# Optimization experiments

Hardware: AMD Instinct MI355X
Metric: run time of the kernel (lower is better)

The kernel has to match this reference:

```python
import jax, jax.numpy as jnp
import numpy as np

H = 1024
NH = 16
HD = H // NH  # 64


def setup_inputs() -> dict:
    key = jax.random.key(0)
    ks = jax.random.split(key, 7)
    s = 1.0 / np.sqrt(H)
    return {
        "hidden_states": jax.random.normal(ks[0], (4, 2048, H), dtype=jnp.float32),
        "Wq": jax.random.normal(ks[1], (H, H), dtype=jnp.float32) * s,
        "bq": jnp.zeros((H,), dtype=jnp.float32),
        "Wk": jax.random.normal(ks[2], (H, H), dtype=jnp.float32) * s,
        "bk": jnp.zeros((H,), dtype=jnp.float32),
        "Wv": jax.random.normal(ks[3], (H, H), dtype=jnp.float32) * s,
        "bv": jnp.zeros((H,), dtype=jnp.float32),
    }


def _split_heads(x):
    # [B,S,H] -> [B,NH,S,HD]
    b, s, _ = x.shape
    return x.reshape(b, s, NH, HD).transpose(0, 2, 1, 3)


def reference(hidden_states, Wq, bq, Wk, bk, Wv, bv):
    q = _split_heads(hidden_states @ Wq + bq)
    k = _split_heads(hidden_states @ Wk + bk)
    v = _split_heads(hidden_states @ Wv + bv)
    scores = jnp.einsum("bhqd,bhkd->bhqk", q, k) / jnp.sqrt(jnp.float32(HD))
    probs = jax.nn.softmax(scores, axis=-1)  # dropout p=0 (eval) -> identity
    ctx = jnp.einsum("bhqk,bhkd->bhqd", probs, v)
    b, _, s, _ = ctx.shape
    return ctx.transpose(0, 2, 1, 3).reshape(b, s, H)
```

## Files before the change

### kernel.cpp

```cpp
#include <hip/hip_runtime.h>
#include <hip/hip_bf16.h>

#define BB  4
#define SS  2048
#define HH  1024
#define NHH 16
#define HDD 64

typedef unsigned short u16;
typedef unsigned int   u32;
using bf16x8 = __attribute__((ext_vector_type(8))) short;
using f32x4  = __attribute__((ext_vector_type(4))) float;
using f32x16 = __attribute__((ext_vector_type(16))) float;
using u32x4  = __attribute__((ext_vector_type(4))) u32;

__device__ __forceinline__ u16 f2b(float f) {
    union { float f; u32 u; } x; x.f = f;
    return (u16)((x.u + 0x7fffu + ((x.u >> 16) & 1u)) >> 16);
}

__device__ __forceinline__ void gload16(const u16* g, u16* l) {
    __builtin_amdgcn_global_load_lds(
        (const __attribute__((address_space(1))) void*)g,
        (__attribute__((address_space(3))) void*)l, 16, 0, 0);
}

__global__ __launch_bounds__(256) void conv(
    const float* __restrict__ X,
    const float* __restrict__ Wq, const float* __restrict__ Wk,
    const float* __restrict__ Wv,
    u16* __restrict__ Xb, u16* __restrict__ Wt)
{
    const int bid = blockIdx.x;
    const int t = threadIdx.x;
    if (bid < 4096) {
        const int i = bid * 256 + t;
        float4 a = ((const float4*)X)[i * 2];
        float4 b = ((const float4*)X)[i * 2 + 1];
        ushort4 s0, s1;
        s0.x = f2b(a.x); s0.y = f2b(a.y); s0.z = f2b(a.z); s0.w = f2b(a.w);
        s1.x = f2b(b.x); s1.y = f2b(b.y); s1.z = f2b(b.z); s1.w = f2b(b.w);
        ((ushort4*)Xb)[i * 2] = s0;
        ((ushort4*)Xb)[i * 2 + 1] = s1;
        return;
    }
    const int idx = bid - 4096;
    const int z = idx >> 10, rem = idx & 1023;
    const int k0 = (rem >> 5) * 32, n0 = (rem & 31) * 32;
    const float* W = (z == 0) ? Wq : (z == 1) ? Wk : Wv;
    u16* out = Wt + (size_t)z * HH * HH;
    __shared__ float T[32][33];
    {
        const int kl = t >> 3, n4 = (t & 7) * 4;
        float4 v = *(const float4*)&W[(size_t)(k0 + kl) * HH + n0 + n4];
        T[n4 + 0][kl] = v.x; T[n4 + 1][kl] = v.y;
        T[n4 + 2][kl] = v.z; T[n4 + 3][kl] = v.w;
    }
    __syncthreads();
    {
        const int nl = t >> 3, k4 = (t & 7) * 4;
        ushort4 s;
        s.x = f2b(T[nl][k4 + 0]); s.y = f2b(T[nl][k4 + 1]);
        s.z = f2b(T[nl][k4 + 2]); s.w = f2b(T[nl][k4 + 3]);
        *(ushort4*)&out[(size_t)(n0 + nl) * HH + k0 + k4] = s;
    }
}

__global__ __launch_bounds__(256) void qkv_gemm(
    const u16* __restrict__ Xb, const u16* __restrict__ Wtb,
    const float* __restrict__ bq, const float* __restrict__ bk,
    const float* __restrict__ bv,
    u16* __restrict__ Qw, u16* __restrict__ Kw, u16* __restrict__ Vw)
{
    const int z  = blockIdx.z;
    const float* bias = (z == 0) ? bq : (z == 1) ? bk : bv;
    const int m0 = blockIdx.x * 128, n0 = blockIdx.y * 128;

    __shared__ __align__(16) u16 Xs[128 * 64];
    __shared__ __align__(16) u16 Ws[128 * 64];

    const int t = threadIdx.x;
    const int w = t >> 6, lane = t & 63, lr = lane & 15, quad = lane >> 4;
    const int l3 = lane >> 3, c7 = lane & 7;
    const int cl = (c7 ^ l3) * 8;
    const int wm = w >> 1, wn = w & 1;

    const u16* Wtz = Wtb + (size_t)z * HH * HH;

    f32x4 acc[4][4];
    #pragma unroll
    for (int i = 0; i < 4; i++)
        #pragma unroll
        for (int j = 0; j < 4; j++) acc[i][j] = f32x4{0.f, 0.f, 0.f, 0.f};

    for (int k0 = 0; k0 < HH; k0 += 64) {
        #pragma unroll
        for (int e = 0; e < 4; e++) {
            const int r = w * 32 + e * 8 + l3;
            gload16(&Xb [(size_t)(m0 + r) * HH + k0 + cl], &Xs[(w * 32 + e * 8) * 64]);
            gload16(&Wtz[(size_t)(n0 + r) * HH + k0 + cl], &Ws[(w * 32 + e * 8) * 64]);
        }
        __syncthreads();

        #pragma unroll
        for (int kc = 0; kc < 2; kc++) {
            bf16x8 af[4], bfr[4];
            const int ph = ((kc * 4 + quad) ^ c7) * 8;
            #pragma unroll
            for (int mi = 0; mi < 4; mi++)
                af[mi] = *(const bf16x8*)&Xs[(wm * 64 + mi * 16 + lr) * 64 + ph];
            #pragma unroll
            for (int ni = 0; ni < 4; ni++)
                bfr[ni] = *(const bf16x8*)&Ws[(wn * 64 + ni * 16 + lr) * 64 + ph];
            if (z != 2) {
                #pragma unroll
                for (int mi = 0; mi < 4; mi++)
                    #pragma unroll
                    for (int ni = 0; ni < 4; ni++)
                        acc[mi][ni] = __builtin_amdgcn_mfma_f32_16x16x32_bf16(
                            bfr[ni], af[mi], acc[mi][ni], 0, 0, 0);
            } else {
                #pragma unroll
                for (int mi = 0; mi < 4; mi++)
                    #pragma unroll
                    for (int ni = 0; ni < 4; ni++)
                        acc[mi][ni] = __builtin_amdgcn_mfma_f32_16x16x32_bf16(
                            af[mi], bfr[ni], acc[mi][ni], 0, 0, 0);
            }
        }
        __syncthreads();
    }

    if (z != 2) {
        u16* dst = (z == 0) ? Qw : Kw;
        const float cs = (z == 0) ? 0.18033688011112042f : 1.0f;
        #pragma unroll
        for (int mi = 0; mi < 4; mi++) {
            const int sg = m0 + wm * 64 + mi * 16 + lr;
            const int b = sg >> 11, s = sg & 2047;
            #pragma unroll
            for (int ni = 0; ni < 4; ni++) {
                const int nb = n0 + wn * 64 + ni * 16 + quad * 4;
                const int h = nb >> 6, d0 = nb & 63;
                float4 bb4 = *(const float4*)&bias[nb];
                ushort4 vs;
                vs.x = f2b((acc[mi][ni][0] + bb4.x) * cs);
                vs.y = f2b((acc[mi][ni][1] + bb4.y) * cs);
                vs.z = f2b((acc[mi][ni][2] + bb4.z) * cs);
                vs.w = f2b((acc[mi][ni][3] + bb4.w) * cs);
                *(ushort4*)&dst[((size_t)(b * NHH + h) * SS + s) * HDD + d0] = vs;
            }
        }
    } else {
        #pragma unroll
        for (int mi = 0; mi < 4; mi++)
            #pragma unroll
            for (int ni = 0; ni < 4; ni++) {
                const int mb = m0 + wm * 64 + mi * 16 + quad * 4;
                const int b = mb >> 11, s0 = mb & 2047;
                const int n = n0 + wn * 64 + ni * 16 + lr;
                const int h = n >> 6, d = n & 63;
                const float bv4 = bias[n];
                ushort4 vs;
                vs.x = f2b(acc[mi][ni][0] + bv4);
                vs.y = f2b(acc[mi][ni][1] + bv4);
                vs.z = f2b(acc[mi][ni][2] + bv4);
                vs.w = f2b(acc[mi][ni][3] + bv4);
                *(ushort4*)&Vw[((size_t)(b * NHH + h) * HDD + d) * SS + s0] = vs;
            }
    }
}

struct PU { union { u32x4 u; bf16x8 v; }; };

__device__ __forceinline__ void packP(const f32x16& s0, const f32x16& s1,
                                      PU pa[4], float& lsum) {
    #pragma unroll
    for (int kb = 0; kb < 2; kb++) {
        const f32x16& s = kb ? s1 : s0;
        float p[16];
        #pragma unroll
        for (int r = 0; r < 16; r++) p[r] = __builtin_amdgcn_exp2f(s[r]);
        lsum += ((((p[0] + p[1]) + (p[2] + p[3]))
                + ((p[4] + p[5]) + (p[6] + p[7])))
               + (((p[8] + p[9]) + (p[10] + p[11]))
                + ((p[12] + p[13]) + (p[14] + p[15]))));
        u32 x0, x1, x2, x3, y0, y1, y2, y3;
        asm("v_cvt_pk_bf16_f32 %0, %1, %2" : "=v"(x0) : "v"(p[0]),  "v"(p[1]));
        asm("v_cvt_pk_bf16_f32 %0, %1, %2" : "=v"(x1) : "v"(p[2]),  "v"(p[3]));
        asm("v_cvt_pk_bf16_f32 %0, %1, %2" : "=v"(y0) : "v"(p[4]),  "v"(p[5]));
        asm("v_cvt_pk_bf16_f32 %0, %1, %2" : "=v"(y1) : "v"(p[6]),  "v"(p[7]));
        asm("v_cvt_pk_bf16_f32 %0, %1, %2" : "=v"(x2) : "v"(p[8]),  "v"(p[9]));
        asm("v_cvt_pk_bf16_f32 %0, %1, %2" : "=v"(x3) : "v"(p[10]), "v"(p[11]));
        asm("v_cvt_pk_bf16_f32 %0, %1, %2" : "=v"(y2) : "v"(p[12]), "v"(p[13]));
        asm("v_cvt_pk_bf16_f32 %0, %1, %2" : "=v"(y3) : "v"(p[14]), "v"(p[15]));
        asm("v_permlane32_swap_b32 %0, %1" : "+v"(x0), "+v"(y0));
        asm("v_permlane32_swap_b32 %0, %1" : "+v"(x1), "+v"(y1));
        asm("v_permlane32_swap_b32 %0, %1" : "+v"(x2), "+v"(y2));
        asm("v_permlane32_swap_b32 %0, %1" : "+v"(x3), "+v"(y3));
        pa[kb * 2 + 0].u = u32x4{x0, x1, y0, y1};
        pa[kb * 2 + 1].u = u32x4{x2, x3, y2, y3};
    }
}

__global__ __launch_bounds__(256, 2) void attn(
    const u16* __restrict__ Qb, const u16* __restrict__ Kb,
    const u16* __restrict__ Vtb, float* __restrict__ Out)
{
    const int bid = blockIdx.x;
    const int hh = bid & 63, qt = bid >> 6;
    const int b = hh >> 4, h = hh & 15;
    const size_t hb = (size_t)hh * SS * HDD;

    __shared__ __align__(16) u16 Ks[2][64 * 64];
    __shared__ __align__(16) u16 Vs[2][64 * 64];

    const int t = threadIdx.x;
    const int w = t >> 6, lane = t & 63;
    const int q32 = lane & 31, hi = lane >> 5;
    const int l3 = lane >> 3, c7 = lane & 7;
    const int cl = (c7 ^ l3) * 8;

    bf16x8 qfA[4], qfB[4];
    {
        const size_t qrA = (size_t)(qt * 256 + w * 64 + q32);
        #pragma unroll
        for (int ds = 0; ds < 4; ds++) {
            qfA[ds] = *(const bf16x8*)&Qb[hb + qrA * HDD + ds * 16 + hi * 8];
            qfB[ds] = *(const bf16x8*)&Qb[hb + (qrA + 32) * HDD + ds * 16 + hi * 8];
        }
    }

    {
        const int r0 = w * 16 + l3, r1 = r0 + 8;
        gload16(&Kb [hb + (size_t)r0 * HDD + cl], &Ks[0][(w * 16) * 64]);
        gload16(&Kb [hb + (size_t)r1 * HDD + cl], &Ks[0][(w * 16 + 8) * 64]);
        gload16(&Vtb[hb + (size_t)r0 * SS + cl],  &Vs[0][(w * 16) * 64]);
        gload16(&Vtb[hb + (size_t)r1 * SS + cl],  &Vs[0][(w * 16 + 8) * 64]);
    }
    __syncthreads();

    float lsA = 0.f, lsB = 0.f;
    f32x16 oA0 = {}, oA1 = {}, oB0 = {}, oB1 = {};

    for (int kt = 0; kt < SS / 64; kt++) {
        const int bb = kt & 1;
        if (kt + 1 < SS / 64) {
            const int r0 = w * 16 + l3, r1 = r0 + 8;
            gload16(&Kb [hb + (size_t)((kt + 1) * 64 + r0) * HDD + cl],
                    &Ks[bb ^ 1][(w * 16) * 64]);
            gload16(&Kb [hb + (size_t)((kt + 1) * 64 + r1) * HDD + cl],
                    &Ks[bb ^ 1][(w * 16 + 8) * 64]);
            gload16(&Vtb[hb + (size_t)r0 * SS + (kt + 1) * 64 + cl],
                    &Vs[bb ^ 1][(w * 16) * 64]);
            gload16(&Vtb[hb + (size_t)r1 * SS + (kt + 1) * 64 + cl],
                    &Vs[bb ^ 1][(w * 16 + 8) * 64]);
        }

        f32x16 sA0 = {}, sA1 = {}, sB0 = {}, sB1 = {};
        __builtin_amdgcn_s_setprio(1);
        #pragma unroll
        for (int ds = 0; ds < 4; ds++) {
            const int ph = ((ds * 2 + hi) ^ c7) * 8;
            bf16x8 kf0 = *(const bf16x8*)&Ks[bb][q32 * 64 + ph];
            bf16x8 kf1 = *(const bf16x8*)&Ks[bb][(32 + q32) * 64 + ph];
            sA0 = __builtin_amdgcn_mfma_f32_32x32x16_bf16(kf0, qfA[ds], sA0, 0, 0, 0);
            sA1 = __builtin_amdgcn_mfma_f32_32x32x16_bf16(kf1, qfA[ds], sA1, 0, 0, 0);
            sB0 = __builtin_amdgcn_mfma_f32_32x32x16_bf16(kf0, qfB[ds], sB0, 0, 0, 0);
            sB1 = __builtin_amdgcn_mfma_f32_32x32x16_bf16(kf1, qfB[ds], sB1, 0, 0, 0);
        }
        __builtin_amdgcn_s_setprio(0);

        PU paA[4], paB[4];
        packP(sA0, sA1, paA, lsA);
        packP(sB0, sB1, paB, lsB);

        __builtin_amdgcn_s_setprio(1);
        #pragma unroll
        for (int ks = 0; ks < 4; ks++) {
            const int ph = ((ks * 2 + hi) ^ c7) * 8;
            bf16x8 vf0 = *(const bf16x8*)&Vs[bb][q32 * 64 + ph];
            bf16x8 vf1 = *(const bf16x8*)&Vs[bb][(32 + q32) * 64 + ph];
            oA0 = __builtin_amdgcn_mfma_f32_32x32x16_bf16(paA[ks].v, vf0, oA0, 0, 0, 0);
            oA1 = __builtin_amdgcn_mfma_f32_32x32x16_bf16(paA[ks].v, vf1, oA1, 0, 0, 0);
            oB0 = __builtin_amdgcn_mfma_f32_32x32x16_bf16(paB[ks].v, vf0, oB0, 0, 0, 0);
            oB1 = __builtin_amdgcn_mfma_f32_32x32x16_bf16(paB[ks].v, vf1, oB1, 0, 0, 0);
        }
        __builtin_amdgcn_s_setprio(0);
        __syncthreads();
    }

    lsA += __shfl_xor(lsA, 32);
    lsB += __shfl_xor(lsB, 32);
    const float invA = 1.0f / lsA, invB = 1.0f / lsB;

    #pragma unroll
    for (int r = 0; r < 16; r++) {
        const int cr = (r & 3) + 8 * (r >> 2) + 4 * hi;
        const float iA = __shfl(invA, cr);
        const float iB = __shfl(invB, cr);
        const int rqA = qt * 256 + w * 64 + cr;
        float* oA = &Out[((size_t)(b * SS + rqA)) * HH + h * HDD + q32];
        oA[0]  = oA0[r] * iA;
        oA[32] = oA1[r] * iA;
        float* oB = &Out[((size_t)(b * SS + rqA + 32)) * HH + h * HDD + q32];
        oB[0]  = oB0[r] * iB;
        oB[32] = oB1[r] * iB;
    }
}

extern "C" void kernel_launch(void* const* d_in, const int* in_sizes, int n_in,
                              void* d_out, int out_size, void* d_ws, size_t ws_size,
                              hipStream_t stream) {
    const float* X  = (const float*)d_in[0];
    const float* Wq = (const float*)d_in[1];
    const float* bq = (const float*)d_in[2];
    const float* Wk = (const float*)d_in[3];
    const float* bk = (const float*)d_in[4];
    const float* Wv = (const float*)d_in[5];
    const float* bv = (const float*)d_in[6];
    float* Out = (float*)d_out;

    const size_t elems = (size_t)BB * SS * HH;
    u16* Qw = (u16*)d_ws;
    u16* Kw = Qw + elems;
    u16* Vw = Kw + elems;
    u16* Xb = (u16*)d_out;
    u16* Wt = Xb + elems;

    conv<<<dim3(4096 + 3072), 256, 0, stream>>>(X, Wq, Wk, Wv, Xb, Wt);
    qkv_gemm<<<dim3(64, 8, 3), 256, 0, stream>>>(Xb, Wt, bq, bk, bv, Qw, Kw, Vw);
    attn<<<dim3(512), 256, 0, stream>>>(Qw, Kw, Vw, Out);
}
```

Measured before the change: 243.5 us.

## Double-buffer QKV GEMM and split attention softmax into interleaved halves

The QKV GEMM gets double-buffered LDS tiles with prefetch of the next k-slice. Each full __syncthreads is replaced by an explicit vmcnt wait plus s_barrier, so the load in flight is not drained at every step. In attention, the score and PV MFMAs are split into two halves so the exp/pack work of one half can overlap MFMA work of the other, and the same partial vmcnt waits are used. This adds 32KB of LDS to the GEMM, relies on hand-counted vmcnt values that must match the number of loads issued, and uses sched barriers that constrain the compiler's scheduling.

```diff
diff --git a/kernel.cpp b/kernel.cpp
--- a/kernel.cpp
+++ b/kernel.cpp
@@ -13,6 +13,12 @@
 using f32x4  = __attribute__((ext_vector_type(4))) float;
 using f32x16 = __attribute__((ext_vector_type(16))) float;
 using u32x4  = __attribute__((ext_vector_type(4))) u32;
+
+#define SBAR()   asm volatile("s_barrier" ::: "memory")
+#define WAITV0() asm volatile("s_waitcnt vmcnt(0)" ::: "memory")
+#define WAITV4() asm volatile("s_waitcnt vmcnt(4)" ::: "memory")
+#define WAITV8() asm volatile("s_waitcnt vmcnt(8)" ::: "memory")
+#define SCHEDB() __builtin_amdgcn_sched_barrier(0)
 
 __device__ __forceinline__ u16 f2b(float f) {
     union { float f; u32 u; } x; x.f = f;
@@ -66,7 +72,7 @@
     }
 }
 
-__global__ __launch_bounds__(256) void qkv_gemm(
+__global__ __launch_bounds__(256, 2) void qkv_gemm(
     const u16* __restrict__ Xb, const u16* __restrict__ Wtb,
     const float* __restrict__ bq, const float* __restrict__ bk,
     const float* __restrict__ bv,
@@ -76,8 +82,8 @@
     const float* bias = (z == 0) ? bq : (z == 1) ? bk : bv;
     const int m0 = blockIdx.x * 128, n0 = blockIdx.y * 128;
 
-    __shared__ __align__(16) u16 Xs[128 * 64];
-    __shared__ __align__(16) u16 Ws[128 * 64];
+    __shared__ __align__(16) u16 Xs[2][128 * 64];
+    __shared__ __align__(16) u16 Ws[2][128 * 64];
 
     const int t = threadIdx.x;
     const int w = t >> 6, lane = t & 63, lr = lane & 15, quad = lane >> 4;
@@ -93,14 +99,31 @@
         #pragma unroll
         for (int j = 0; j < 4; j++) acc[i][j] = f32x4{0.f, 0.f, 0.f, 0.f};
 
-    for (int k0 = 0; k0 < HH; k0 += 64) {
-        #pragma unroll
-        for (int e = 0; e < 4; e++) {
-            const int r = w * 32 + e * 8 + l3;
-            gload16(&Xb [(size_t)(m0 + r) * HH + k0 + cl], &Xs[(w * 32 + e * 8) * 64]);
-            gload16(&Wtz[(size_t)(n0 + r) * HH + k0 + cl], &Ws[(w * 32 + e * 8) * 64]);
-        }
-        __syncthreads();
+    #pragma unroll
+    for (int e = 0; e < 4; e++) {
+        const int r = w * 32 + e * 8 + l3;
+        gload16(&Xb [(size_t)(m0 + r) * HH + cl], &Xs[0][(w * 32 + e * 8) * 64]);
+        gload16(&Wtz[(size_t)(n0 + r) * HH + cl], &Ws[0][(w * 32 + e * 8) * 64]);
+    }
+
+    for (int kt = 0; kt < 16; kt++) {
+        const int cur = kt & 1;
+        if (kt < 15) {
+            const int k0 = (kt + 1) * 64;
+            #pragma unroll
+            for (int e = 0; e < 4; e++) {
+                const int r = w * 32 + e * 8 + l3;
+                gload16(&Xb [(size_t)(m0 + r) * HH + k0 + cl],
+                        &Xs[cur ^ 1][(w * 32 + e * 8) * 64]);
+                gload16(&Wtz[(size_t)(n0 + r) * HH + k0 + cl],
+                        &Ws[cur ^ 1][(w * 32 + e * 8) * 64]);
+            }
+            WAITV8();
+        } else {
+            WAITV0();
+        }
+        SBAR();
+        SCHEDB();
 
         #pragma unroll
         for (int kc = 0; kc < 2; kc++) {
@@ -108,10 +131,10 @@
             const int ph = ((kc * 4 + quad) ^ c7) * 8;
             #pragma unroll
             for (int mi = 0; mi < 4; mi++)
-                af[mi] = *(const bf16x8*)&Xs[(wm * 64 + mi * 16 + lr) * 64 + ph];
+                af[mi] = *(const bf16x8*)&Xs[cur][(wm * 64 + mi * 16 + lr) * 64 + ph];
             #pragma unroll
             for (int ni = 0; ni < 4; ni++)
-                bfr[ni] = *(const bf16x8*)&Ws[(wn * 64 + ni * 16 + lr) * 64 + ph];
+                bfr[ni] = *(const bf16x8*)&Ws[cur][(wn * 64 + ni * 16 + lr) * 64 + ph];
             if (z != 2) {
                 #pragma unroll
                 for (int mi = 0; mi < 4; mi++)
@@ -128,7 +151,8 @@
                             af[mi], bfr[ni], acc[mi][ni], 0, 0, 0);
             }
         }
-        __syncthreads();
+        SCHEDB();
+        SBAR();
     }
 
     if (z != 2) {
@@ -173,34 +197,29 @@
 
 struct PU { union { u32x4 u; bf16x8 v; }; };
 
-__device__ __forceinline__ void packP(const f32x16& s0, const f32x16& s1,
-                                      PU pa[4], float& lsum) {
+__device__ __forceinline__ void packHalf(const f32x16& s, PU* pa, float& lsum) {
+    float p[16];
     #pragma unroll
-    for (int kb = 0; kb < 2; kb++) {
-        const f32x16& s = kb ? s1 : s0;
-        float p[16];
-        #pragma unroll
-        for (int r = 0; r < 16; r++) p[r] = __builtin_amdgcn_exp2f(s[r]);
-        lsum += ((((p[0] + p[1]) + (p[2] + p[3]))
-                + ((p[4] + p[5]) + (p[6] + p[7])))
-               + (((p[8] + p[9]) + (p[10] + p[11]))
-                + ((p[12] + p[13]) + (p[14] + p[15]))));
-        u32 x0, x1, x2, x3, y0, y1, y2, y3;
-        asm("v_cvt_pk_bf16_f32 %0, %1, %2" : "=v"(x0) : "v"(p[0]),  "v"(p[1]));
-        asm("v_cvt_pk_bf16_f32 %0, %1, %2" : "=v"(x1) : "v"(p[2]),  "v"(p[3]));
-        asm("v_cvt_pk_bf16_f32 %0, %1, %2" : "=v"(y0) : "v"(p[4]),  "v"(p[5]));
-        asm("v_cvt_pk_bf16_f32 %0, %1, %2" : "=v"(y1) : "v"(p[6]),  "v"(p[7]));
-        asm("v_cvt_pk_bf16_f32 %0, %1, %2" : "=v"(x2) : "v"(p[8]),  "v"(p[9]));
-        asm("v_cvt_pk_bf16_f32 %0, %1, %2" : "=v"(x3) : "v"(p[10]), "v"(p[11]));
-        asm("v_cvt_pk_bf16_f32 %0, %1, %2" : "=v"(y2) : "v"(p[12]), "v"(p[13]));
-        asm("v_cvt_pk_bf16_f32 %0, %1, %2" : "=v"(y3) : "v"(p[14]), "v"(p[15]));
-        asm("v_permlane32_swap_b32 %0, %1" : "+v"(x0), "+v"(y0));
-        asm("v_permlane32_swap_b32 %0, %1" : "+v"(x1), "+v"(y1));
-        asm("v_permlane32_swap_b32 %0, %1" : "+v"(x2), "+v"(y2));
-        asm("v_permlane32_swap_b32 %0, %1" : "+v"(x3), "+v"(y3));
-        pa[kb * 2 + 0].u = u32x4{x0, x1, y0, y1};
-        pa[kb * 2 + 1].u = u32x4{x2, x3, y2, y3};
-    }
+    for (int r = 0; r < 16; r++) p[r] = __builtin_amdgcn_exp2f(s[r]);
+    lsum += ((((p[0] + p[1]) + (p[2] + p[3]))
+            + ((p[4] + p[5]) + (p[6] + p[7])))
+           + (((p[8] + p[9]) + (p[10] + p[11]))
+            + ((p[12] + p[13]) + (p[14] + p[15]))));
+    u32 x0, x1, x2, x3, y0, y1, y2, y3;
+    asm("v_cvt_pk_bf16_f32 %0, %1, %2" : "=v"(x0) : "v"(p[0]),  "v"(p[1]));
+    asm("v_cvt_pk_bf16_f32 %0, %1, %2" : "=v"(x1) : "v"(p[2]),  "v"(p[3]));
+    asm("v_cvt_pk_bf16_f32 %0, %1, %2" : "=v"(y0) : "v"(p[4]),  "v"(p[5]));
+    asm("v_cvt_pk_bf16_f32 %0, %1, %2" : "=v"(y1) : "v"(p[6]),  "v"(p[7]));
+    asm("v_cvt_pk_bf16_f32 %0, %1, %2" : "=v"(x2) : "v"(p[8]),  "v"(p[9]));
+    asm("v_cvt_pk_bf16_f32 %0, %1, %2" : "=v"(x3) : "v"(p[10]), "v"(p[11]));
+    asm("v_cvt_pk_bf16_f32 %0, %1, %2" : "=v"(y2) : "v"(p[12]), "v"(p[13]));
+    asm("v_cvt_pk_bf16_f32 %0, %1, %2" : "=v"(y3) : "v"(p[14]), "v"(p[15]));
+    asm("v_permlane32_swap_b32 %0, %1" : "+v"(x0), "+v"(y0));
+    asm("v_permlane32_swap_b32 %0, %1" : "+v"(x1), "+v"(y1));
+    asm("v_permlane32_swap_b32 %0, %1" : "+v"(x2), "+v"(y2));
+    asm("v_permlane32_swap_b32 %0, %1" : "+v"(x3), "+v"(y3));
+    pa[0].u = u32x4{x0, x1, y0, y1};
+    pa[1].u = u32x4{x2, x3, y2, y3};
 }
 
 __global__ __launch_bounds__(256, 2) void attn(
@@ -230,6 +249,8 @@
             qfB[ds] = *(const bf16x8*)&Qb[hb + (qrA + 32) * HDD + ds * 16 + hi * 8];
         }
     }
+    asm volatile("" :: "v"(qfA[0]), "v"(qfA[1]), "v"(qfA[2]), "v"(qfA[3]),
+                       "v"(qfB[0]), "v"(qfB[1]), "v"(qfB[2]), "v"(qfB[3]));
 
     {
         const int r0 = w * 16 + l3, r1 = r0 + 8;
@@ -238,7 +259,6 @@
         gload16(&Vtb[hb + (size_t)r0 * SS + cl],  &Vs[0][(w * 16) * 64]);
         gload16(&Vtb[hb + (size_t)r1 * SS + cl],  &Vs[0][(w * 16 + 8) * 64]);
     }
-    __syncthreads();
 
     float lsA = 0.f, lsB = 0.f;
     f32x16 oA0 = {}, oA1 = {}, oB0 = {}, oB1 = {};
@@ -255,29 +275,39 @@
                     &Vs[bb ^ 1][(w * 16) * 64]);
             gload16(&Vtb[hb + (size_t)r1 * SS + (kt + 1) * 64 + cl],
                     &Vs[bb ^ 1][(w * 16 + 8) * 64]);
-        }
-
-        f32x16 sA0 = {}, sA1 = {}, sB0 = {}, sB1 = {};
+            WAITV4();
+        } else {
+            WAITV0();
+        }
+        SBAR();
+        SCHEDB();
+
+        f32x16 sA0 = {}, sB0 = {};
         __builtin_amdgcn_s_setprio(1);
         #pragma unroll
         for (int ds = 0; ds < 4; ds++) {
             const int ph = ((ds * 2 + hi) ^ c7) * 8;
-            bf16x8 kf0 = *(const bf16x8*)&Ks[bb][q32 * 64 + ph];
-            bf16x8 kf1 = *(const bf16x8*)&Ks[bb][(32 + q32) * 64 + ph];
-            sA0 = __builtin_amdgcn_mfma_f32_32x32x16_bf16(kf0, qfA[ds], sA0, 0, 0, 0);
-            sA1 = __builtin_amdgcn_mfma_f32_32x32x16_bf16(kf1, qfA[ds], sA1, 0, 0, 0);
-            sB0 = __builtin_amdgcn_mfma_f32_32x32x16_bf16(kf0, qfB[ds], sB0, 0, 0, 0);
-            sB1 = __builtin_amdgcn_mfma_f32_32x32x16_bf16(kf1, qfB[ds], sB1, 0, 0, 0);
+            bf16x8 kf = *(const bf16x8*)&Ks[bb][q32 * 64 + ph];
+            sA0 = __builtin_amdgcn_mfma_f32_32x32x16_bf16(kf, qfA[ds], sA0, 0, 0, 0);
+            sB0 = __builtin_amdgcn_mfma_f32_32x32x16_bf16(kf, qfB[ds], sB0, 0, 0, 0);
+        }
+        f32x16 sA1 = {}, sB1 = {};
+        #pragma unroll
+        for (int ds = 0; ds < 4; ds++) {
+            const int ph = ((ds * 2 + hi) ^ c7) * 8;
+            bf16x8 kf = *(const bf16x8*)&Ks[bb][(32 + q32) * 64 + ph];
+            sA1 = __builtin_amdgcn_mfma_f32_32x32x16_bf16(kf, qfA[ds], sA1, 0, 0, 0);
+            sB1 = __builtin_amdgcn_mfma_f32_32x32x16_bf16(kf, qfB[ds], sB1, 0, 0, 0);
         }
         __builtin_amdgcn_s_setprio(0);
 
         PU paA[4], paB[4];
-        packP(sA0, sA1, paA, lsA);
-        packP(sB0, sB1, paB, lsB);
+        packHalf(sA0, &paA[0], lsA);
+        packHalf(sB0, &paB[0], lsB);
 
         __builtin_amdgcn_s_setprio(1);
         #pragma unroll
-        for (int ks = 0; ks < 4; ks++) {
+        for (int ks = 0; ks < 2; ks++) {
             const int ph = ((ks * 2 + hi) ^ c7) * 8;
             bf16x8 vf0 = *(const bf16x8*)&Vs[bb][q32 * 64 + ph];
             bf16x8 vf1 = *(const bf16x8*)&Vs[bb][(32 + q32) * 64 + ph];
@@ -287,7 +317,25 @@
             oB1 = __builtin_amdgcn_mfma_f32_32x32x16_bf16(paB[ks].v, vf1, oB1, 0, 0, 0);
         }
         __builtin_amdgcn_s_setprio(0);
-        __syncthreads();
+
+        packHalf(sA1, &paA[2], lsA);
+        packHalf(sB1, &paB[2], lsB);
+
+        __builtin_amdgcn_s_setprio(1);
+        #pragma unroll
+        for (int ks = 2; ks < 4; ks++) {
+            const int ph = ((ks * 2 + hi) ^ c7) * 8;
+            bf16x8 vf0 = *(const bf16x8*)&Vs[bb][q32 * 64 + ph];
+            bf16x8 vf1 = *(const bf16x8*)&Vs[bb][(32 + q32) * 64 + ph];
+            oA0 = __builtin_amdgcn_mfma_f32_32x32x16_bf16(paA[ks].v, vf0, oA0, 0, 0, 0);
+            oA1 = __builtin_amdgcn_mfma_f32_32x32x16_bf16(paA[ks].v, vf1, oA1, 0, 0, 0);
+            oB0 = __builtin_amdgcn_mfma_f32_32x32x16_bf16(paB[ks].v, vf0, oB0, 0, 0, 0);
+            oB1 = __builtin_amdgcn_mfma_f32_32x32x16_bf16(paB[ks].v, vf1, oB1, 0, 0, 0);
+        }
+        __builtin_amdgcn_s_setprio(0);
+
+        SCHEDB();
+        SBAR();
     }
 
     lsA += __shfl_xor(lsA, 32);
```

New measurement: 245.2 us. No clear change (+0.7%).
